# Performance work log

Hardware: AMD Instinct MI355X
Metric: run time of the kernel (lower is better)

The kernel has to match this reference:

```python
import jax, jax.numpy as jnp
import numpy as np

B, N, DIM, H = 2, 2048, 1024, 16
D = DIM // H  # head_dim = 64


def setup_inputs() -> dict:
    key = jax.random.key(0)
    ks = jax.random.split(key, 3)
    w_scale = 0.02
    return {
        "x": jax.random.normal(ks[0], (B, N, DIM), dtype=jnp.float32),
        "Wqkv": jax.random.normal(ks[1], (DIM, 3 * DIM), dtype=jnp.float32) * w_scale,
        "bqkv": jnp.zeros((3 * DIM,), dtype=jnp.float32),
        "Wproj": jax.random.normal(ks[2], (DIM, DIM), dtype=jnp.float32) * w_scale,
        "bproj": jnp.zeros((DIM,), dtype=jnp.float32),
        "sigma": jnp.ones((1,), dtype=jnp.float32),
        "gamma": jnp.ones((1,), dtype=jnp.float32),
    }


def reference(x, Wqkv, bqkv, Wproj, bproj, sigma, gamma):
    b, n, c = x.shape
    # qkv projection -> (B, N, 3, H, D)
    qkv = (x @ Wqkv + bqkv).reshape(b, n, 3, H, D)
    q = jnp.transpose(qkv[:, :, 0], (0, 2, 1, 3))  # [B, H, N, D]
    k = jnp.transpose(qkv[:, :, 1], (0, 2, 1, 3))
    v = jnp.transpose(qkv[:, :, 2], (0, 2, 1, 3))
    scale = 1.0 / jnp.sqrt(jnp.asarray(D, dtype=x.dtype))
    scores = jnp.einsum("bhqd,bhkd->bhqk", q, k) * scale  # [B, H, N, N]
    # divisive normalization (cortical gain control) over key axis
    denom = sigma + jnp.sqrt(jnp.mean(scores * scores, axis=-1, keepdims=True))
    scores = gamma * scores / denom
    attn = jax.nn.softmax(scores, axis=-1)
    out = jnp.einsum("bhqk,bhkd->bhqd", attn, v)  # [B, H, N, D]
    out = jnp.transpose(out, (0, 2, 1, 3)).reshape(b, n, c)
    return out @ Wproj + bproj
```

## Files before the change

kernel.cpp:

```cpp
#include <hip/hip_runtime.h>

typedef __attribute__((ext_vector_type(4))) float f32x4;
typedef __attribute__((ext_vector_type(8))) _Float16 f16x8;
typedef __attribute__((ext_vector_type(4))) _Float16 f16x4;

#define MFMA_F16(a, b, c) __builtin_amdgcn_mfma_f32_16x16x32_f16(a, b, c, 0, 0, 0)

__device__ __forceinline__ void gload_lds16(const void* g, void* l) {
  __builtin_amdgcn_global_load_lds(
      (const __attribute__((address_space(1))) void*)g,
      (__attribute__((address_space(3))) void*)l, 16, 0, 0);
}

__global__ __launch_bounds__(256) void cast_x_kernel(
    const float* __restrict__ x, _Float16* __restrict__ xf, int n4) {
  int i = blockIdx.x * 256 + threadIdx.x;
  if (i >= n4) return;
  f32x4 v = *(const f32x4*)(x + (size_t)i * 4);
  f16x4 h;
#pragma unroll
  for (int j = 0; j < 4; ++j) h[j] = (_Float16)v[j];
  *(f16x4*)(xf + (size_t)i * 4) = h;
}

__global__ __launch_bounds__(256) void transpose_w_kernel(
    const float* __restrict__ W, _Float16* __restrict__ wt, int K, int N) {
  __shared__ float tile[32][33];
  const int n0 = blockIdx.x * 32, k0 = blockIdx.y * 32;
  const int tx = threadIdx.x & 31, ty = threadIdx.x >> 5;
#pragma unroll
  for (int j = 0; j < 32; j += 8)
    tile[ty + j][tx] = W[(size_t)(k0 + ty + j) * N + n0 + tx];
  __syncthreads();
#pragma unroll
  for (int j = 0; j < 32; j += 8)
    wt[(size_t)(n0 + ty + j) * K + k0 + tx] = (_Float16)tile[tx][ty + j];
}

__global__ __launch_bounds__(256) void gemm_qkv_kernel(
    const _Float16* __restrict__ xf, const _Float16* __restrict__ wt,
    const float* __restrict__ bias, _Float16* __restrict__ QF,
    _Float16* __restrict__ KF, _Float16* __restrict__ KT,
    _Float16* __restrict__ VT) {
  __shared__ __attribute__((aligned(16))) _Float16 lg[16512];
  const int tid = threadIdx.x, lane = tid & 63, w = tid >> 6;
  const int m0 = blockIdx.y * 128, n0 = blockIdx.x * 128;
  const int wr = (w >> 1) * 64, wc = (w & 1) * 64;
  f32x4 acc[4][4] = {};

  const int srow = lane >> 2;
  const int scol = (((lane & 3) ^ ((lane >> 3) & 3)) * 8);
  const int fr = lane & 15, fg = lane >> 4;
  const int rswz = (fr >> 1) & 3;

  for (int k0 = 0; k0 < 1024; k0 += 32) {
#pragma unroll
    for (int j = 0; j < 2; ++j) {
      const int rbase = 32 * w + 16 * j;
      const int r = rbase + srow;
      gload_lds16(xf + (size_t)(m0 + r) * 1024 + k0 + scol, &lg[rbase * 32]);
      gload_lds16(wt + (size_t)(n0 + r) * 1024 + k0 + scol, &lg[4096 + rbase * 32]);
    }
    __syncthreads();
    f16x8 af[4], bfr[4];
#pragma unroll
    for (int m = 0; m < 4; ++m)
      af[m] = *(const f16x8*)&lg[(wr + 16 * m + fr) * 32 + ((fg ^ rswz) * 8)];
#pragma unroll
    for (int n = 0; n < 4; ++n)
      bfr[n] = *(const f16x8*)&lg[4096 + (wc + 16 * n + fr) * 32 + ((fg ^ rswz) * 8)];
#pragma unroll
    for (int m = 0; m < 4; ++m)
#pragma unroll
      for (int n = 0; n < 4; ++n) acc[m][n] = MFMA_F16(af[m], bfr[n], acc[m][n]);
    __syncthreads();
  }

  const int fq = fg * 4;
#pragma unroll
  for (int n = 0; n < 4; ++n) {
    const float bv = bias[n0 + wc + 16 * n + fr];
#pragma unroll
    for (int m = 0; m < 4; ++m)
#pragma unroll
      for (int i = 0; i < 4; ++i)
        lg[(wr + 16 * m + fq + i) * 129 + wc + 16 * n + fr] =
            (_Float16)(acc[m][n][i] + bv);
  }
  __syncthreads();
  const int b = m0 >> 11, nnb = m0 & 2047;
  const int h0 = 2 * (blockIdx.x & 7);
  const int sPhase = blockIdx.x >> 3;
  if (sPhase <= 1) {
    _Float16* __restrict__ dst = (sPhase == 0) ? QF : KF;
#pragma unroll
    for (int p = 0; p < 8; ++p) {
      const int r = p * 16 + (tid >> 4);
      const int c = tid & 15;
      f16x8 vals;
#pragma unroll
      for (int j = 0; j < 8; ++j) vals[j] = lg[r * 129 + c * 8 + j];
      const int h = c >> 3, d = (c & 7) * 8;
      *(f16x8*)&dst[((size_t)((b * 16 + h0 + h) * 2048 + nnb + r)) * 64 + d] = vals;
    }
  }
  if (sPhase >= 1) {
    _Float16* __restrict__ T = (sPhase == 1) ? KT : VT;
#pragma unroll
    for (int p = 0; p < 8; ++p) {
      const int lr = p * 16 + (tid >> 4);
      const int cc = tid & 15;
      f16x8 vals;
#pragma unroll
      for (int j = 0; j < 8; ++j) vals[j] = lg[(cc * 8 + j) * 129 + lr];
      const int h = lr >> 6, d = lr & 63;
      *(f16x8*)&T[((size_t)((b * 16 + h0 + h) * 64 + d)) * 2048 + nnb + cc * 8] = vals;
    }
  }
}

__global__ __launch_bounds__(256) void gram_kernel(
    const _Float16* __restrict__ KT, _Float16* __restrict__ GH,
    _Float16* __restrict__ GL) {
  __shared__ __attribute__((aligned(16))) _Float16 sT[2][4096];
  const int tid = threadIdx.x, lane = tid & 63, w = tid >> 6;
  const int bh = blockIdx.x;
  const _Float16* src = KT + (size_t)bh * 64 * 2048;
  const int s_r = lane >> 3, s_cg = lane & 7;
  const int fr = lane & 15, fg = lane >> 4;
  const int kswz = fr & 7;

  auto stage = [&](int buf, int n0) {
#pragma unroll
    for (int j = 0; j < 2; ++j) {
      const int rbase = 8 * w + 32 * j;
      gload_lds16(src + (size_t)(rbase + s_r) * 2048 + n0 + ((s_cg ^ s_r) * 8),
                  &sT[buf][rbase * 64]);
    }
  };

  f32x4 acc[4] = {};
  stage(0, 0);
  __syncthreads();
  for (int t = 0; t < 32; ++t) {
    const int cur = t & 1;
    if (t < 31) stage(cur ^ 1, (t + 1) * 64);
    f16x8 af[2];
#pragma unroll
    for (int ks = 0; ks < 2; ++ks)
      af[ks] = *(const f16x8*)&sT[cur][(16 * w + fr) * 64 + (((ks * 4 + fg) ^ kswz) * 8)];
#pragma unroll
    for (int nt = 0; nt < 4; ++nt)
#pragma unroll
      for (int ks = 0; ks < 2; ++ks)
        acc[nt] = MFMA_F16(
            af[ks],
            *(const f16x8*)&sT[cur][(16 * nt + fr) * 64 + (((ks * 4 + fg) ^ kswz) * 8)],
            acc[nt]);
    __syncthreads();
  }
#pragma unroll
  for (int nt = 0; nt < 4; ++nt) {
#pragma unroll
    for (int i = 0; i < 4; ++i) {
      const float g = acc[nt][i];
      const _Float16 gh = (_Float16)g;
      const size_t o = (size_t)bh * 4096 + (16 * w + fg * 4 + i) * 64 + 16 * nt + fr;
      GH[o] = gh;
      GL[o] = (_Float16)(g - (float)gh);
    }
  }
}

__global__ __launch_bounds__(256) void attn_kernel(
    const _Float16* __restrict__ QF, const _Float16* __restrict__ KF,
    const _Float16* __restrict__ VT, const _Float16* __restrict__ GH,
    const _Float16* __restrict__ GL, _Float16* __restrict__ OB,
    const float* __restrict__ sigma_p, const float* __restrict__ gamma_p) {
  __shared__ __attribute__((aligned(16))) _Float16 lds[16384];

  const int tid = threadIdx.x, lane = tid & 63, w = tid >> 6;
  const int bh = blockIdx.y;
  const int q0 = blockIdx.x * 128;
  const size_t base = (size_t)bh * (2048 * 64);
  const float sigma = sigma_p[0], gamma = gamma_p[0];
  const int fr = lane & 15, fg = lane >> 4;
  const int s_r = lane >> 3, s_cg = lane & 7;
  const int kswz = fr & 7;

  const _Float16* Kbh = KF + base;
  const _Float16* Tbh = VT + base;

  f16x8 qf[2][2];
#pragma unroll
  for (int m = 0; m < 2; ++m)
#pragma unroll
    for (int ks = 0; ks < 2; ++ks)
      qf[m][ks] = *(const f16x8*)(QF + base +
                                  (size_t)(q0 + 32 * w + 16 * m + fr) * 64 +
                                  ks * 32 + fg * 8);

  auto stage64 = [&](int dstoff, const _Float16* g, int srcstride) {
#pragma unroll
    for (int j = 0; j < 2; ++j) {
      const int rbase = 8 * w + 32 * j;
      gload_lds16(g + (size_t)(rbase + s_r) * srcstride + ((s_cg ^ s_r) * 8),
                  &lds[dstoff + rbase * 64]);
    }
  };
  auto stage64K = [&](int dstoff, const _Float16* g) {
#pragma unroll
    for (int j = 0; j < 2; ++j) {
      const int rbase = 8 * w + 32 * j;
      const int r = rbase + s_r;
      const int pr = (r & 0x23) | ((r & 0x0C) << 1) | ((r & 0x10) >> 2);
      gload_lds16(g + (size_t)pr * 64 + ((s_cg ^ s_r) * 8),
                  &lds[dstoff + rbase * 64]);
    }
  };

  stage64(0, GH + (size_t)bh * 4096, 64);
  stage64(4096, GL + (size_t)bh * 4096, 64);
  __syncthreads();
  float minvl2[2];
  float* Yp = (float*)&lds[8192 + w * 2048];
#pragma unroll
  for (int m = 0; m < 2; ++m) {
    f32x4 yacc[4] = {};
#pragma unroll
    for (int nt = 0; nt < 4; ++nt) {
#pragma unroll
      for (int ks = 0; ks < 2; ++ks) {
        const int off = (16 * nt + fr) * 64 + (((ks * 4 + fg) ^ kswz) * 8);
        yacc[nt] = MFMA_F16(qf[m][ks], *(const f16x8*)&lds[off], yacc[nt]);
        yacc[nt] = MFMA_F16(qf[m][ks], *(const f16x8*)&lds[4096 + off], yacc[nt]);
      }
    }
#pragma unroll
    for (int nt = 0; nt < 4; ++nt)
#pragma unroll
      for (int i = 0; i < 4; ++i) Yp[(fg * 4 + i) * 64 + 16 * nt + fr] = yacc[nt][i];
    float zp = 0.0f;
#pragma unroll
    for (int ks = 0; ks < 2; ++ks) {
      const f32x4 y0 = *(const f32x4*)&Yp[fr * 64 + ks * 32 + fg * 8];
      const f32x4 y1 = *(const f32x4*)&Yp[fr * 64 + ks * 32 + fg * 8 + 4];
#pragma unroll
      for (int c = 0; c < 4; ++c) {
        zp += y0[c] * (float)qf[m][ks][c];
        zp += y1[c] * (float)qf[m][ks][c + 4];
      }
    }
    zp += __shfl_xor(zp, 16);
    zp += __shfl_xor(zp, 32);
    const float rms = sqrtf(fmaxf(zp, 0.0f)) * (1.0f / 362.038672f);
    minvl2[m] = gamma / (sigma + rms) * 0.125f * 1.44269504f;
  }
  __syncthreads();

  float lsum[2] = {};
  f32x4 oacc[2][4] = {};
  stage64K(0, Kbh);
  stage64(8192, Tbh, 2048);
  __syncthreads();
  for (int kb = 0; kb < 32; ++kb) {
    const int cur = kb & 1;
    if (kb < 31) {
      stage64K((cur ^ 1) * 4096, Kbh + (size_t)(kb + 1) * 64 * 64);
      stage64(8192 + (cur ^ 1) * 4096, Tbh + (kb + 1) * 64, 2048);
    }
    f32x4 pacc[2][4];
#pragma unroll
    for (int n = 0; n < 4; ++n) {
      const int offb = cur * 4096 + (16 * n + fr) * 64;
      const f16x8 kf0 = *(const f16x8*)&lds[offb + ((fg ^ kswz) * 8)];
      const f16x8 kf1 = *(const f16x8*)&lds[offb + (((4 + fg) ^ kswz) * 8)];
#pragma unroll
      for (int m = 0; m < 2; ++m) {
        f32x4 a = {};
        a = MFMA_F16(kf0, qf[m][0], a);
        a = MFMA_F16(kf1, qf[m][1], a);
        pacc[m][n] = a;
      }
    }
#pragma unroll
    for (int m = 0; m < 2; ++m)
#pragma unroll
      for (int n = 0; n < 4; ++n)
#pragma unroll
        for (int i = 0; i < 4; ++i) {
          const float p = __builtin_amdgcn_exp2f(pacc[m][n][i] * minvl2[m]);
          lsum[m] += p;
          pacc[m][n][i] = p;
        }
#pragma unroll
    for (int ks2 = 0; ks2 < 2; ++ks2) {
      f16x8 bf[2];
#pragma unroll
      for (int m = 0; m < 2; ++m) {
        bf[m][0] = (_Float16)pacc[m][2 * ks2][0];
        bf[m][1] = (_Float16)pacc[m][2 * ks2][1];
        bf[m][2] = (_Float16)pacc[m][2 * ks2][2];
        bf[m][3] = (_Float16)pacc[m][2 * ks2][3];
        bf[m][4] = (_Float16)pacc[m][2 * ks2 + 1][0];
        bf[m][5] = (_Float16)pacc[m][2 * ks2 + 1][1];
        bf[m][6] = (_Float16)pacc[m][2 * ks2 + 1][2];
        bf[m][7] = (_Float16)pacc[m][2 * ks2 + 1][3];
      }
#pragma unroll
      for (int nf = 0; nf < 4; ++nf) {
        const int off = 8192 + cur * 4096 + (16 * nf + fr) * 64 +
                        (((ks2 * 4 + fg) ^ kswz) * 8);
        const f16x8 vt = *(const f16x8*)&lds[off];
        oacc[0][nf] = MFMA_F16(vt, bf[0], oacc[0][nf]);
        oacc[1][nf] = MFMA_F16(vt, bf[1], oacc[1][nf]);
      }
    }
    __syncthreads();
  }
  float inv[2];
#pragma unroll
  for (int m = 0; m < 2; ++m) {
    lsum[m] += __shfl_xor(lsum[m], 16);
    lsum[m] += __shfl_xor(lsum[m], 32);
    inv[m] = 1.0f / lsum[m];
  }

  const int b = bh >> 4, h = bh & 15;
#pragma unroll
  for (int m = 0; m < 2; ++m) {
    const size_t orow = (size_t)(b * 2048 + q0 + 32 * w + 16 * m + fr);
#pragma unroll
    for (int nf = 0; nf < 4; ++nf) {
      f16x4 ov;
#pragma unroll
      for (int i = 0; i < 4; ++i) ov[i] = (_Float16)(oacc[m][nf][i] * inv[m]);
      *(f16x4*)&OB[orow * 1024 + h * 64 + 16 * nf + 4 * fg] = ov;
    }
  }
}

__global__ __launch_bounds__(256) void gemm_proj_kernel(
    const _Float16* __restrict__ A, const _Float16* __restrict__ Bt,
    const float* __restrict__ bias, float* __restrict__ out) {
  __shared__ __attribute__((aligned(16))) _Float16 sA[128 * 32];
  __shared__ __attribute__((aligned(16))) _Float16 sB[128 * 32];
  const int tid = threadIdx.x, lane = tid & 63, w = tid >> 6;
  const int m0 = blockIdx.y * 128, n0 = blockIdx.x * 128;
  const int wr = (w >> 1) * 64, wc = (w & 1) * 64;
  f32x4 acc[4][4] = {};
  const int srow = lane >> 2;
  const int scol = (((lane & 3) ^ ((lane >> 3) & 3)) * 8);
  const int fr = lane & 15, fg = lane >> 4;
  const int rswz = (fr >> 1) & 3;

  for (int k0 = 0; k0 < 1024; k0 += 32) {
#pragma unroll
    for (int j = 0; j < 2; ++j) {
      const int rbase = 32 * w + 16 * j;
      const int r = rbase + srow;
      gload_lds16(A + (size_t)(m0 + r) * 1024 + k0 + scol, &sA[rbase * 32]);
      gload_lds16(Bt + (size_t)(n0 + r) * 1024 + k0 + scol, &sB[rbase * 32]);
    }
    __syncthreads();
    f16x8 af[4], bfr[4];
#pragma unroll
    for (int m = 0; m < 4; ++m)
      af[m] = *(const f16x8*)&sA[(wr + 16 * m + fr) * 32 + ((fg ^ rswz) * 8)];
#pragma unroll
    for (int n = 0; n < 4; ++n)
      bfr[n] = *(const f16x8*)&sB[(wc + 16 * n + fr) * 32 + ((fg ^ rswz) * 8)];
#pragma unroll
    for (int m = 0; m < 4; ++m)
#pragma unroll
      for (int n = 0; n < 4; ++n) acc[m][n] = MFMA_F16(af[m], bfr[n], acc[m][n]);
    __syncthreads();
  }
  const int fq = fg * 4;
#pragma unroll
  for (int n = 0; n < 4; ++n) {
    const int col = n0 + wc + 16 * n + fr;
    const float bv = bias[col];
#pragma unroll
    for (int m = 0; m < 4; ++m) {
#pragma unroll
      for (int i = 0; i < 4; ++i) {
        const int row = m0 + wr + 16 * m + fq + i;
        out[(size_t)row * 1024 + col] = acc[m][n][i] + bv;
      }
    }
  }
}

extern "C" void kernel_launch(void* const* d_in, const int* in_sizes, int n_in,
                              void* d_out, int out_size, void* d_ws, size_t ws_size,
                              hipStream_t stream) {
  const float* x = (const float*)d_in[0];
  const float* Wqkv = (const float*)d_in[1];
  const float* bqkv = (const float*)d_in[2];
  const float* Wproj = (const float*)d_in[3];
  const float* bproj = (const float*)d_in[4];
  const float* sigma = (const float*)d_in[5];
  const float* gamma = (const float*)d_in[6];
  float* out = (float*)d_out;

  char* ws = (char*)d_ws;
  const size_t MB = 1024 * 1024;
  _Float16* XF  = (_Float16*)(ws + 0 * MB);
  _Float16* WQT = (_Float16*)(ws + 8 * MB);
  _Float16* WPT = (_Float16*)(ws + 14 * MB);
  _Float16* QF  = (_Float16*)(ws + 16 * MB);
  _Float16* KF  = (_Float16*)(ws + 24 * MB);
  _Float16* VT  = (_Float16*)(ws + 32 * MB);
  _Float16* KT  = (_Float16*)(ws + 40 * MB);
  _Float16* OB  = (_Float16*)(ws + 40 * MB);
  _Float16* GH  = (_Float16*)(ws + 8 * MB);
  _Float16* GL  = (_Float16*)(ws + 8 * MB + 512 * 1024);

  cast_x_kernel<<<4096, 256, 0, stream>>>(x, XF, 1048576);
  transpose_w_kernel<<<dim3(96, 32), 256, 0, stream>>>(Wqkv, WQT, 1024, 3072);
  transpose_w_kernel<<<dim3(32, 32), 256, 0, stream>>>(Wproj, WPT, 1024, 1024);
  gemm_qkv_kernel<<<dim3(24, 32), 256, 0, stream>>>(XF, WQT, bqkv, QF, KF, KT, VT);
  gram_kernel<<<32, 256, 0, stream>>>(KT, GH, GL);
  attn_kernel<<<dim3(16, 32), 256, 0, stream>>>(QF, KF, VT, GH, GL, OB, sigma, gamma);
  gemm_proj_kernel<<<dim3(8, 32), 256, 0, stream>>>(OB, WPT, bproj, out);
}
```

Measured before the change: 142.6 us.

## Triple-buffer LDS staging with partial vmcnt barriers in GEMMs and attention

Converts the QKV GEMM, projection GEMM and attention K/V loops to a three-stage LDS ring buffer. Each iteration prefetches two tiles ahead and waits with s_waitcnt vmcnt(4) instead of a full __syncthreads, so global-to-LDS loads for future tiles stay in flight during MFMA work. The QKV GEMM previously had no prefetch; the attention loop was double-buffered. It also packs the fp32-to-fp16 probability conversion with cvt_pkrtz, which rounds toward zero. LDS use rises to 48 KB per block, which may cut occupancy, and the vmcnt(4) count depends on exactly four loads issued per stage.

```diff
diff --git a/kernel.cpp b/kernel.cpp
--- a/kernel.cpp
+++ b/kernel.cpp
@@ -3,6 +3,7 @@
 typedef __attribute__((ext_vector_type(4))) float f32x4;
 typedef __attribute__((ext_vector_type(8))) _Float16 f16x8;
 typedef __attribute__((ext_vector_type(4))) _Float16 f16x4;
+typedef __attribute__((ext_vector_type(2))) _Float16 f16x2;
 
 #define MFMA_F16(a, b, c) __builtin_amdgcn_mfma_f32_16x16x32_f16(a, b, c, 0, 0, 0)
 
@@ -10,6 +11,19 @@
   __builtin_amdgcn_global_load_lds(
       (const __attribute__((address_space(1))) void*)g,
       (__attribute__((address_space(3))) void*)l, 16, 0, 0);
+}
+__device__ __forceinline__ f16x2 pk2(float a, float b) {
+  return __builtin_bit_cast(f16x2, __builtin_amdgcn_cvt_pkrtz(a, b));
+}
+__device__ __forceinline__ void pipe_barrier_v4() {
+  asm volatile("s_waitcnt vmcnt(4) lgkmcnt(0)" ::: "memory");
+  __builtin_amdgcn_sched_barrier(0);
+  __builtin_amdgcn_s_barrier();
+}
+__device__ __forceinline__ void pipe_barrier_v0() {
+  asm volatile("s_waitcnt vmcnt(0) lgkmcnt(0)" ::: "memory");
+  __builtin_amdgcn_sched_barrier(0);
+  __builtin_amdgcn_s_barrier();
 }
 
 __global__ __launch_bounds__(256) void cast_x_kernel(
@@ -42,7 +56,7 @@
     const float* __restrict__ bias, _Float16* __restrict__ QF,
     _Float16* __restrict__ KF, _Float16* __restrict__ KT,
     _Float16* __restrict__ VT) {
-  __shared__ __attribute__((aligned(16))) _Float16 lg[16512];
+  __shared__ __attribute__((aligned(16))) _Float16 lg[24576];
   const int tid = threadIdx.x, lane = tid & 63, w = tid >> 6;
   const int m0 = blockIdx.y * 128, n0 = blockIdx.x * 128;
   const int wr = (w >> 1) * 64, wc = (w & 1) * 64;
@@ -53,27 +67,41 @@
   const int fr = lane & 15, fg = lane >> 4;
   const int rswz = (fr >> 1) & 3;
 
-  for (int k0 = 0; k0 < 1024; k0 += 32) {
+  auto stageT = [&](int buf, int k0) {
 #pragma unroll
     for (int j = 0; j < 2; ++j) {
       const int rbase = 32 * w + 16 * j;
       const int r = rbase + srow;
-      gload_lds16(xf + (size_t)(m0 + r) * 1024 + k0 + scol, &lg[rbase * 32]);
-      gload_lds16(wt + (size_t)(n0 + r) * 1024 + k0 + scol, &lg[4096 + rbase * 32]);
-    }
-    __syncthreads();
+      gload_lds16(xf + (size_t)(m0 + r) * 1024 + k0 + scol,
+                  &lg[buf * 8192 + rbase * 32]);
+      gload_lds16(wt + (size_t)(n0 + r) * 1024 + k0 + scol,
+                  &lg[buf * 8192 + 4096 + rbase * 32]);
+    }
+  };
+
+  stageT(0, 0);
+  stageT(1, 32);
+  pipe_barrier_v4();
+  int cur = 0;
+  for (int t = 0; t < 32; ++t) {
+    if (t < 30) {
+      const int nb = (cur + 2 >= 3) ? cur - 1 : cur + 2;
+      stageT(nb, (t + 2) * 32);
+    }
+    const int ab = cur * 8192;
     f16x8 af[4], bfr[4];
 #pragma unroll
     for (int m = 0; m < 4; ++m)
-      af[m] = *(const f16x8*)&lg[(wr + 16 * m + fr) * 32 + ((fg ^ rswz) * 8)];
+      af[m] = *(const f16x8*)&lg[ab + (wr + 16 * m + fr) * 32 + ((fg ^ rswz) * 8)];
 #pragma unroll
     for (int n = 0; n < 4; ++n)
-      bfr[n] = *(const f16x8*)&lg[4096 + (wc + 16 * n + fr) * 32 + ((fg ^ rswz) * 8)];
+      bfr[n] = *(const f16x8*)&lg[ab + 4096 + (wc + 16 * n + fr) * 32 + ((fg ^ rswz) * 8)];
 #pragma unroll
     for (int m = 0; m < 4; ++m)
 #pragma unroll
       for (int n = 0; n < 4; ++n) acc[m][n] = MFMA_F16(af[m], bfr[n], acc[m][n]);
-    __syncthreads();
+    if (t < 30) pipe_barrier_v4(); else pipe_barrier_v0();
+    cur = (cur + 1 == 3) ? 0 : cur + 1;
   }
 
   const int fq = fg * 4;
@@ -177,7 +205,7 @@
     const _Float16* __restrict__ VT, const _Float16* __restrict__ GH,
     const _Float16* __restrict__ GL, _Float16* __restrict__ OB,
     const float* __restrict__ sigma_p, const float* __restrict__ gamma_p) {
-  __shared__ __attribute__((aligned(16))) _Float16 lds[16384];
+  __shared__ __attribute__((aligned(16))) _Float16 lds[24576];
 
   const int tid = threadIdx.x, lane = tid & 63, w = tid >> 6;
   const int bh = blockIdx.y;
@@ -261,18 +289,22 @@
   float lsum[2] = {};
   f32x4 oacc[2][4] = {};
   stage64K(0, Kbh);
-  stage64(8192, Tbh, 2048);
-  __syncthreads();
+  stage64(12288, Tbh, 2048);
+  stage64K(4096, Kbh + 64 * 64);
+  stage64(16384, Tbh + 64, 2048);
+  pipe_barrier_v4();
+  int cur = 0;
   for (int kb = 0; kb < 32; ++kb) {
-    const int cur = kb & 1;
-    if (kb < 31) {
-      stage64K((cur ^ 1) * 4096, Kbh + (size_t)(kb + 1) * 64 * 64);
-      stage64(8192 + (cur ^ 1) * 4096, Tbh + (kb + 1) * 64, 2048);
-    }
+    if (kb < 30) {
+      const int nb = (cur + 2 >= 3) ? cur - 1 : cur + 2;
+      stage64K(nb * 4096, Kbh + (size_t)(kb + 2) * 64 * 64);
+      stage64(12288 + nb * 4096, Tbh + (kb + 2) * 64, 2048);
+    }
+    const int koff = cur * 4096, voff = 12288 + cur * 4096;
     f32x4 pacc[2][4];
 #pragma unroll
     for (int n = 0; n < 4; ++n) {
-      const int offb = cur * 4096 + (16 * n + fr) * 64;
+      const int offb = koff + (16 * n + fr) * 64;
       const f16x8 kf0 = *(const f16x8*)&lds[offb + ((fg ^ kswz) * 8)];
       const f16x8 kf1 = *(const f16x8*)&lds[offb + (((4 + fg) ^ kswz) * 8)];
 #pragma unroll
@@ -298,25 +330,23 @@
       f16x8 bf[2];
 #pragma unroll
       for (int m = 0; m < 2; ++m) {
-        bf[m][0] = (_Float16)pacc[m][2 * ks2][0];
-        bf[m][1] = (_Float16)pacc[m][2 * ks2][1];
-        bf[m][2] = (_Float16)pacc[m][2 * ks2][2];
-        bf[m][3] = (_Float16)pacc[m][2 * ks2][3];
-        bf[m][4] = (_Float16)pacc[m][2 * ks2 + 1][0];
-        bf[m][5] = (_Float16)pacc[m][2 * ks2 + 1][1];
-        bf[m][6] = (_Float16)pacc[m][2 * ks2 + 1][2];
-        bf[m][7] = (_Float16)pacc[m][2 * ks2 + 1][3];
+        const f16x2 c0 = pk2(pacc[m][2 * ks2][0], pacc[m][2 * ks2][1]);
+        const f16x2 c1 = pk2(pacc[m][2 * ks2][2], pacc[m][2 * ks2][3]);
+        const f16x2 c2 = pk2(pacc[m][2 * ks2 + 1][0], pacc[m][2 * ks2 + 1][1]);
+        const f16x2 c3 = pk2(pacc[m][2 * ks2 + 1][2], pacc[m][2 * ks2 + 1][3]);
+        bf[m][0] = c0[0]; bf[m][1] = c0[1]; bf[m][2] = c1[0]; bf[m][3] = c1[1];
+        bf[m][4] = c2[0]; bf[m][5] = c2[1]; bf[m][6] = c3[0]; bf[m][7] = c3[1];
       }
 #pragma unroll
       for (int nf = 0; nf < 4; ++nf) {
-        const int off = 8192 + cur * 4096 + (16 * nf + fr) * 64 +
-                        (((ks2 * 4 + fg) ^ kswz) * 8);
+        const int off = voff + (16 * nf + fr) * 64 + (((ks2 * 4 + fg) ^ kswz) * 8);
         const f16x8 vt = *(const f16x8*)&lds[off];
         oacc[0][nf] = MFMA_F16(vt, bf[0], oacc[0][nf]);
         oacc[1][nf] = MFMA_F16(vt, bf[1], oacc[1][nf]);
       }
     }
-    __syncthreads();
+    if (kb < 30) pipe_barrier_v4(); else pipe_barrier_v0();
+    cur = (cur + 1 == 3) ? 0 : cur + 1;
   }
   float inv[2];
 #pragma unroll
@@ -343,8 +373,7 @@
 __global__ __launch_bounds__(256) void gemm_proj_kernel(
     const _Float16* __restrict__ A, const _Float16* __restrict__ Bt,
     const float* __restrict__ bias, float* __restrict__ out) {
-  __shared__ __attribute__((aligned(16))) _Float16 sA[128 * 32];
-  __shared__ __attribute__((aligned(16))) _Float16 sB[128 * 32];
+  __shared__ __attribute__((aligned(16))) _Float16 lg[24576];
   const int tid = threadIdx.x, lane = tid & 63, w = tid >> 6;
   const int m0 = blockIdx.y * 128, n0 = blockIdx.x * 128;
   const int wr = (w >> 1) * 64, wc = (w & 1) * 64;
@@ -354,27 +383,41 @@
   const int fr = lane & 15, fg = lane >> 4;
   const int rswz = (fr >> 1) & 3;
 
-  for (int k0 = 0; k0 < 1024; k0 += 32) {
+  auto stageT = [&](int buf, int k0) {
 #pragma unroll
     for (int j = 0; j < 2; ++j) {
       const int rbase = 32 * w + 16 * j;
       const int r = rbase + srow;
-      gload_lds16(A + (size_t)(m0 + r) * 1024 + k0 + scol, &sA[rbase * 32]);
-      gload_lds16(Bt + (size_t)(n0 + r) * 1024 + k0 + scol, &sB[rbase * 32]);
-    }
-    __syncthreads();
+      gload_lds16(A + (size_t)(m0 + r) * 1024 + k0 + scol,
+                  &lg[buf * 8192 + rbase * 32]);
+      gload_lds16(Bt + (size_t)(n0 + r) * 1024 + k0 + scol,
+                  &lg[buf * 8192 + 4096 + rbase * 32]);
+    }
+  };
+
+  stageT(0, 0);
+  stageT(1, 32);
+  pipe_barrier_v4();
+  int cur = 0;
+  for (int t = 0; t < 32; ++t) {
+    if (t < 30) {
+      const int nb = (cur + 2 >= 3) ? cur - 1 : cur + 2;
+      stageT(nb, (t + 2) * 32);
+    }
+    const int ab = cur * 8192;
     f16x8 af[4], bfr[4];
 #pragma unroll
     for (int m = 0; m < 4; ++m)
-      af[m] = *(const f16x8*)&sA[(wr + 16 * m + fr) * 32 + ((fg ^ rswz) * 8)];
+      af[m] = *(const f16x8*)&lg[ab + (wr + 16 * m + fr) * 32 + ((fg ^ rswz) * 8)];
 #pragma unroll
     for (int n = 0; n < 4; ++n)
-      bfr[n] = *(const f16x8*)&sB[(wc + 16 * n + fr) * 32 + ((fg ^ rswz) * 8)];
+      bfr[n] = *(const f16x8*)&lg[ab + 4096 + (wc + 16 * n + fr) * 32 + ((fg ^ rswz) * 8)];
 #pragma unroll
     for (int m = 0; m < 4; ++m)
 #pragma unroll
       for (int n = 0; n < 4; ++n) acc[m][n] = MFMA_F16(af[m], bfr[n], acc[m][n]);
-    __syncthreads();
+    if (t < 30) pipe_barrier_v4(); else pipe_barrier_v0();
+    cur = (cur + 1 == 3) ? 0 : cur + 1;
   }
   const int fq = fg * 4;
 #pragma unroll
```

Result: faster. 133.7 us (-6.2%).
